# Kernel optimization log

Hardware: AMD Instinct MI355X
Metric: run time of the kernel (lower is better)

The kernel has to match this reference:

```python
import jax, jax.numpy as jnp
import numpy as np

B, N, D, H, E, K = 8, 1024, 768, 12, 4, 9
PAD = (K - 1) // 2


def _ln(x, g, b, eps=1e-5):
    m = jnp.mean(x, -1, keepdims=True)
    v = jnp.var(x, -1, keepdims=True)
    return (x - m) * jax.lax.rsqrt(v + eps) * g + b


def setup_inputs() -> dict:
    key = jax.random.key(0)
    ks = jax.random.split(key, 12)
    w = lambda k, s: jax.random.normal(k, s, jnp.float32) * 0.02
    return {
        "x": jax.random.normal(ks[0], (B, N, D), jnp.float32),
        "ff1_ln_g": jnp.ones(D), "ff1_ln_b": jnp.zeros(D),
        "ff1_w1": w(ks[1], (D, E * D)), "ff1_b1": jnp.zeros(E * D),
        "ff1_w2": w(ks[2], (E * D, D)), "ff1_b2": jnp.zeros(D),
        "attn_ln_g": jnp.ones(D), "attn_ln_b": jnp.zeros(D),
        "qkv_w": w(ks[3], (D, 3 * D)), "qkv_b": jnp.zeros(3 * D),
        "proj_w": w(ks[4], (D, D)), "proj_b": jnp.zeros(D),
        "rel_table": w(ks[5], (2 * N - 1, H)),
        "conv_ln_g": jnp.ones(D), "conv_ln_b": jnp.zeros(D),
        "pwin_w": w(ks[6], (2 * D, D)), "pwin_b": jnp.zeros(2 * D),
        "dw_w": w(ks[7], (D, 1, K)), "dw_b": jnp.zeros(D),
        "bn_g": jnp.ones(D), "bn_b": jnp.zeros(D),
        "pwout_w": w(ks[8], (D, D)), "pwout_b": jnp.zeros(D),
        "ff2_ln_g": jnp.ones(D), "ff2_ln_b": jnp.zeros(D),
        "ff2_w1": w(ks[9], (D, E * D)), "ff2_b1": jnp.zeros(E * D),
        "ff2_w2": w(ks[10], (E * D, D)), "ff2_b2": jnp.zeros(D),
        "fin_ln_g": jnp.ones(D), "fin_ln_b": jnp.zeros(D),
    }


def _ffn(x, g, b, w1, b1, w2, b2):
    h = jax.nn.gelu(_ln(x, g, b) @ w1 + b1, approximate=False)
    return h @ w2 + b2


def _attn(x, qkv_w, qkv_b, proj_w, proj_b, rel_table):
    b_, n_, c = x.shape
    hd = c // H
    qkv = (x @ qkv_w + qkv_b).reshape(b_, n_, 3, H, hd).transpose(2, 0, 3, 1, 4)
    q, k, v = qkv[0], qkv[1], qkv[2]  # (B, H, N, hd)
    scores = jnp.einsum('bhqd,bhkd->bhqk', q, k) * (hd ** -0.5)
    coords = jnp.arange(n_)
    idx = coords[None, :] - coords[:, None] + N - 1  # (N, N) in [0, 2N-2]
    bias = rel_table[idx].transpose(2, 0, 1)  # (H, N, N)
    a = jax.nn.softmax(scores + bias[None], axis=-1)
    out = jnp.einsum('bhqk,bhkd->bhqd', a, v).transpose(0, 2, 1, 3).reshape(b_, n_, c)
    return out @ proj_w + proj_b


def _conv(x, g, b, pwin_w, pwin_b, dw_w, dw_b, bn_g, bn_b, pwout_w, pwout_b):
    y = _ln(x, g, b) @ pwin_w.T + pwin_b  # pointwise-in conv as matmul -> (B, N, 2D)
    u, gate = jnp.split(y, 2, axis=-1)
    y = (u * jax.nn.sigmoid(gate)).transpose(0, 2, 1)  # GLU over channels -> (B, D, N)
    y = jax.lax.conv_general_dilated(
        y, dw_w, (1,), [(PAD, PAD)], feature_group_count=D,
        dimension_numbers=('NCH', 'OIH', 'NCH')) + dw_b[None, :, None]
    m = jnp.mean(y, (0, 2), keepdims=True)  # BatchNorm1d, training-mode batch stats
    v = jnp.var(y, (0, 2), keepdims=True)
    y = (y - m) * jax.lax.rsqrt(v + 1e-5) * bn_g[None, :, None] + bn_b[None, :, None]
    y = y * jax.nn.sigmoid(y)  # SiLU
    y = jnp.einsum('bcn,oc->bno', y, pwout_w) + pwout_b  # pointwise-out, back to (B, N, D)
    return y


def reference(x, ff1_ln_g, ff1_ln_b, ff1_w1, ff1_b1, ff1_w2, ff1_b2,
              attn_ln_g, attn_ln_b, qkv_w, qkv_b, proj_w, proj_b, rel_table,
              conv_ln_g, conv_ln_b, pwin_w, pwin_b, dw_w, dw_b, bn_g, bn_b,
              pwout_w, pwout_b, ff2_ln_g, ff2_ln_b, ff2_w1, ff2_b1, ff2_w2, ff2_b2,
              fin_ln_g, fin_ln_b):
    x = x + 0.5 * _ffn(x, ff1_ln_g, ff1_ln_b, ff1_w1, ff1_b1, ff1_w2, ff1_b2)
    x = x + _attn(_ln(x, attn_ln_g, attn_ln_b), qkv_w, qkv_b, proj_w, proj_b, rel_table)
    x = x + _conv(x, conv_ln_g, conv_ln_b, pwin_w, pwin_b, dw_w, dw_b, bn_g, bn_b, pwout_w, pwout_b)
    x = x + 0.5 * _ffn(x, ff2_ln_g, ff2_ln_b, ff2_w1, ff2_b1, ff2_w2, ff2_b2)
    return _ln(x, fin_ln_g, fin_ln_b)
```

## Files before the change

### kernel.cpp

```cpp
#include <hip/hip_runtime.h>
#include <math.h>

#define Bb 8
#define Nn 1024
#define Dd 768
#define Hh 12
#define Mm 8192

typedef __attribute__((ext_vector_type(4))) float f32x4;
typedef __attribute__((ext_vector_type(8))) __bf16 bf16x8;

__device__ __forceinline__ float bf2f(unsigned short u) {
  union { unsigned int i; float f; } v; v.i = ((unsigned int)u) << 16; return v.f;
}
__device__ __forceinline__ unsigned short f2bf(float f) {
  union { float f; unsigned int i; } v; v.f = f;
  unsigned int u = v.i;
  return (unsigned short)((u + 0x7FFFu + ((u >> 16) & 1u)) >> 16);
}
__device__ __forceinline__ unsigned int pack2bf(float a, float b) {
  union { __bf16 h[2]; unsigned int u; } x;
  x.h[0] = (__bf16)a; x.h[1] = (__bf16)b; return x.u;
}

__device__ __forceinline__ void gload16(const void* g, void* l) {
  __builtin_amdgcn_global_load_lds(
      (const __attribute__((address_space(1))) unsigned int*)g,
      (__attribute__((address_space(3))) unsigned int*)l, 16, 0, 0);
}

__device__ __forceinline__ float gelu_f(float v) {
  const float z = fabsf(v) * 0.7071067811865475f;
  const float t = __builtin_amdgcn_rcpf(1.f + 0.3275911f * z);
  const float poly = t*(0.254829592f + t*(-0.284496736f + t*(1.421413741f +
                     t*(-1.453152027f + t*1.061405429f))));
  float er = 1.f - poly * __expf(-z * z);
  er = copysignf(er, v);
  return 0.5f * v * (1.f + er);
}

template<int EPI, int NT>
__global__ __launch_bounds__(256)
void gemm_bt(const unsigned short* __restrict__ A,
             const unsigned short* __restrict__ Bt,
             const float* __restrict__ bias,
             unsigned short* __restrict__ Cbf,
             float* __restrict__ Res,
             const float* __restrict__ Xin,
             unsigned short* __restrict__ Vtr,
             int M, int N, int K, float scale)
{
  __shared__ __align__(16) unsigned short Asm[128*64];
  __shared__ __align__(16) unsigned short Bsm[NT*64];
  const int tid = threadIdx.x;
  const int wv = tid >> 6, lane = tid & 63;
  const int lr = lane & 15, lg = lane >> 4;
  const int wr = wv >> 1, wc = wv & 1;
  constexpr int JN = NT / 32;

  const int gx = gridDim.x, gy = gridDim.y;
  const int nwg = gx * gy;
  const int lin = blockIdx.y * gx + blockIdx.x;
  const int q8 = nwg >> 3, r8 = nwg & 7;
  const int xcd = lin & 7, lidx = lin >> 3;
  const int wg = ((xcd < r8) ? xcd * (q8 + 1) : r8 * (q8 + 1) + (xcd - r8) * q8) + lidx;
  const int bx = wg % gx;
  const int by = wg / gx;

  const int n0 = bx * NT, m0 = by * 128;

  f32x4 acc[4][JN] = {};

  const int srow8 = lane >> 3;
  const int scol  = ((lane & 7) ^ srow8) * 8;
  const unsigned short* Agp = A + (size_t)(m0 + wv*32 + srow8)*K + scol;
  const unsigned short* Bgp = (NT == 128)
      ? Bt + (size_t)(n0 + wv*32 + srow8)*K + scol
      : Bt + (size_t)(n0 + wv*16 + srow8)*K + scol;
  const int swr = (lr & 7) << 4;

  for (int kt = 0; kt < K; kt += 64) {
#pragma unroll
    for (int k = 0; k < 4; k++)
      gload16(Agp + (size_t)(k*8)*K + kt, Asm + (wv*32 + k*8)*64);
    if (NT == 128) {
#pragma unroll
      for (int k = 0; k < 4; k++)
        gload16(Bgp + (size_t)(k*8)*K + kt, Bsm + (wv*32 + k*8)*64);
    } else {
#pragma unroll
      for (int k = 0; k < 2; k++)
        gload16(Bgp + (size_t)(k*8)*K + kt, Bsm + (wv*16 + k*8)*64);
    }
    __syncthreads();
    bf16x8 af[4], af2[4], bfr[JN], bfr2[JN];
#pragma unroll
    for (int i = 0; i < 4; i++) {
      const char* base = (const char*)Asm + (wr*64 + i*16 + lr)*128;
      af[i]  = *(const bf16x8*)(base + ((lg*16)      ^ swr));
      af2[i] = *(const bf16x8*)(base + ((lg*16 + 64) ^ swr));
    }
#pragma unroll
    for (int j = 0; j < JN; j++) {
      const char* base = (const char*)Bsm + (wc*(NT/2) + j*16 + lr)*128;
      bfr[j]  = *(const bf16x8*)(base + ((lg*16)      ^ swr));
      bfr2[j] = *(const bf16x8*)(base + ((lg*16 + 64) ^ swr));
    }
#pragma unroll
    for (int i = 0; i < 4; i++)
#pragma unroll
      for (int j = 0; j < JN; j++) {
        acc[i][j] = __builtin_amdgcn_mfma_f32_16x16x32_bf16(af[i],  bfr[j],  acc[i][j], 0, 0, 0);
        acc[i][j] = __builtin_amdgcn_mfma_f32_16x16x32_bf16(af2[i], bfr2[j], acc[i][j], 0, 0, 0);
      }
    __syncthreads();
  }

#pragma unroll
  for (int i = 0; i < 4; i++) {
    const int rg = m0 + wr*64 + i*16 + lg*4;
    if (EPI == 3) {
#pragma unroll
      for (int j = 0; j < JN; j += 2) {
        const int cgu = n0 + wc*(NT/2) + j*16 + lr;
        const float bu = bias[cgu], bg = bias[cgu + 16];
        const int ocol = (n0 >> 1) + wc*(NT/4) + (j >> 1)*16 + lr;
#pragma unroll
        for (int e = 0; e < 4; e++) {
          float u  = acc[i][j][e]   + bu;
          float gt = acc[i][j+1][e] + bg;
          Cbf[(size_t)(rg + e) * (N >> 1) + ocol] = f2bf(u / (1.f + __expf(-gt)));
        }
      }
    } else if (EPI == 5 && n0 >= 1536) {
#pragma unroll
      for (int j = 0; j < JN; j++) {
        const int cg = n0 + wc*(NT/2) + j*16 + lr;
        const float bv = bias[cg];
        const int vo = cg - 1536;
        const int hh = vo >> 6, d = vo & 63;
        const int bb_ = rg >> 10, nn_ = rg & 1023;
        ushort4 o4;
        o4.x = f2bf(acc[i][j][0] + bv);
        o4.y = f2bf(acc[i][j][1] + bv);
        o4.z = f2bf(acc[i][j][2] + bv);
        o4.w = f2bf(acc[i][j][3] + bv);
        *(ushort4*)(Vtr + (((size_t)bb_*Hh + hh)*64 + d)*1024 + nn_) = o4;
      }
    } else {
#pragma unroll
      for (int j = 0; j < JN; j++) {
        const int cg = n0 + wc*(NT/2) + j*16 + lr;
        const float bv = bias[cg];
#pragma unroll
        for (int e = 0; e < 4; e++) {
          float v = acc[i][j][e] + bv;
          const size_t idx = (size_t)(rg + e) * N + cg;
          if (EPI == 1) {
            Cbf[idx] = f2bf(gelu_f(v));
          } else if (EPI == 0 || EPI == 5) {
            Cbf[idx] = f2bf(v);
          } else if (EPI == 2) {
            Res[idx] += scale * v;
          } else {
            Res[idx] = Xin[idx] + scale * v;
          }
        }
      }
    }
  }
}

template<bool OBF>
__global__ __launch_bounds__(256)
void ln_kernel(const float* x, const float* __restrict__ g,
               const float* __restrict__ b, void* out)
{
  const int row = blockIdx.x, tid = threadIdx.x;
  const float* xr = x + (size_t)row * Dd;
  float v0 = xr[tid], v1 = xr[tid+256], v2 = xr[tid+512];
  float s = v0+v1+v2, q = v0*v0+v1*v1+v2*v2;
  for (int off = 32; off; off >>= 1) { s += __shfl_down(s, off); q += __shfl_down(q, off); }
  __shared__ float ps[4], pq[4];
  if ((tid & 63) == 0) { ps[tid>>6] = s; pq[tid>>6] = q; }
  __syncthreads();
  s = ps[0]+ps[1]+ps[2]+ps[3]; q = pq[0]+pq[1]+pq[2]+pq[3];
  const float mean = s * (1.f/768.f);
  const float rstd = rsqrtf(q*(1.f/768.f) - mean*mean + 1e-5f);
  float y0 = (v0-mean)*rstd*g[tid]     + b[tid];
  float y1 = (v1-mean)*rstd*g[tid+256] + b[tid+256];
  float y2 = (v2-mean)*rstd*g[tid+512] + b[tid+512];
  if (OBF) {
    unsigned short* o = (unsigned short*)out + (size_t)row * Dd;
    o[tid] = f2bf(y0); o[tid+256] = f2bf(y1); o[tid+512] = f2bf(y2);
  } else {
    float* o = (float*)out + (size_t)row * Dd;
    o[tid] = y0; o[tid+256] = y1; o[tid+512] = y2;
  }
}

__global__ __launch_bounds__(256)
void transpose_w(const float* __restrict__ src, unsigned short* __restrict__ dst,
                 int K, int N)
{
  __shared__ float t[32][33];
  const int tx = threadIdx.x, ty = threadIdx.y;
  const int n0 = blockIdx.x * 32, k0 = blockIdx.y * 32;
#pragma unroll
  for (int i = 0; i < 4; i++) t[ty + i*8][tx] = src[(size_t)(k0 + ty + i*8)*N + n0 + tx];
  __syncthreads();
#pragma unroll
  for (int i = 0; i < 4; i++)
    dst[(size_t)(n0 + ty + i*8)*K + k0 + tx] = f2bf(t[tx][ty + i*8]);
}

__global__ __launch_bounds__(256)
void convert_bf(const float* __restrict__ src, unsigned short* __restrict__ dst, int n)
{
  for (int i = blockIdx.x*256 + threadIdx.x; i < n; i += gridDim.x*256)
    dst[i] = f2bf(src[i]);
}

__global__ __launch_bounds__(256)
void perm_pwin(const float* __restrict__ w, const float* __restrict__ b,
               unsigned short* __restrict__ wt, float* __restrict__ bperm)
{
  const int r = blockIdx.x;
  const int blk = r >> 7, g = (r >> 4) & 7, t = r & 15;
  const int orig = blk*64 + ((g >> 1) << 4) + t + ((g & 1) ? 768 : 0);
  const float* src = w + (size_t)orig * 768;
  unsigned short* dst = wt + (size_t)r * 768;
  const int tid = threadIdx.x;
  dst[tid] = f2bf(src[tid]); dst[tid+256] = f2bf(src[tid+256]); dst[tid+512] = f2bf(src[tid+512]);
  if (tid == 0) bperm[r] = b[orig];
}

__global__ __launch_bounds__(256)
void dw_tr(const float* __restrict__ src, float* __restrict__ dst)
{
  const int id = blockIdx.x*256 + threadIdx.x;
  if (id >= 9*768) return;
  const int k = id / 768, d = id % 768;
  dst[id] = src[d*9 + k];
}

__global__ __launch_bounds__(256)
void attn_kernel(const unsigned short* __restrict__ qkv,
                 const unsigned short* __restrict__ vtr,
                 const float* __restrict__ rel,
                 unsigned short* __restrict__ out)
{
  const int bh = blockIdx.x; const int b = bh / Hh, h = bh % Hh;
  const int q0 = blockIdx.y * 64;
  const int tid = threadIdx.x, wv = tid >> 6, lane = tid & 63;
  const int lr = lane & 15, lg = lane >> 4;

  __shared__ __align__(16) unsigned short Kl[64*72];
  __shared__ __align__(16) unsigned short Vt[64*72 + 64];
  __shared__ __align__(16) unsigned short Pl[4*16*72];
  __shared__ float relh[2048];

  for (int i = tid; i < 2047; i += 256) relh[i] = rel[(size_t)i*Hh + h] * 1.44269504f;

  const size_t qrow = (size_t)(b*Nn + q0 + wv*16 + lr);
  const bf16x8 qraw0 = *(const bf16x8*)(qkv + qrow*2304 + h*64 + lg*8);
  const bf16x8 qraw1 = *(const bf16x8*)(qkv + qrow*2304 + h*64 + 32 + lg*8);
  bf16x8 qf0, qf1;
#pragma unroll
  for (int e = 0; e < 8; e++) {
    qf0[e] = (__bf16)((float)qraw0[e] * 0.180336884f);
    qf1[e] = (__bf16)((float)qraw1[e] * 0.180336884f);
  }

  const int sd = tid >> 2;
  const int sc = (tid & 3) * 16;
  unsigned short* Pw = Pl + wv*16*72;

  const unsigned short* kbase = qkv + (size_t)(b*Nn + sd)*2304 + 768 + h*64 + sc;
  const unsigned short* vbase = vtr + ((size_t)bh*64 + sd)*Nn + sc;
  bf16x8 kA = *(const bf16x8*)(kbase);
  bf16x8 kB = *(const bf16x8*)(kbase + 8);
  bf16x8 vA = *(const bf16x8*)(vbase);
  bf16x8 vB = *(const bf16x8*)(vbase + 8);

  f32x4 O[4] = {};
  float mrow = -1e30f, lsum = 0.f;
  const int qq = q0 + wv*16 + lr;

  __syncthreads();

  for (int kt = 0; kt < Nn; kt += 64) {
    {
      *(bf16x8*)&Kl[sd*72 + sc]     = kA;
      *(bf16x8*)&Kl[sd*72 + sc + 8] = kB;
      const int vb_ = sd*72 + (sd>>4)*16 + sc;
      *(bf16x8*)&Vt[vb_]     = vA;
      *(bf16x8*)&Vt[vb_ + 8] = vB;
    }
    __syncthreads();

    if (kt + 64 < Nn) {
      const unsigned short* kn = kbase + (size_t)(kt + 64)*2304;
      const unsigned short* vn = vbase + (kt + 64);
      kA = *(const bf16x8*)(kn);
      kB = *(const bf16x8*)(kn + 8);
      vA = *(const bf16x8*)(vn);
      vB = *(const bf16x8*)(vn + 8);
    }

    f32x4 s[4] = {};
#pragma unroll
    for (int kb = 0; kb < 4; kb++) {
      bf16x8 kfa = *(const bf16x8*)&Kl[(kb*16 + lr)*72 + lg*8];
      bf16x8 kfb = *(const bf16x8*)&Kl[(kb*16 + lr)*72 + 32 + lg*8];
      s[kb] = __builtin_amdgcn_mfma_f32_16x16x32_bf16(kfa, qf0, s[kb], 0, 0, 0);
      s[kb] = __builtin_amdgcn_mfma_f32_16x16x32_bf16(kfb, qf1, s[kb], 0, 0, 0);
    }

    const int bidx = kt - qq + (Nn - 1);
    float v[4][4]; float r = -1e30f;
#pragma unroll
    for (int kb = 0; kb < 4; kb++)
#pragma unroll
      for (int j = 0; j < 4; j++) {
        float t = s[kb][j] + relh[bidx + kb*16 + lg*4 + j];
        v[kb][j] = t; r = fmaxf(r, t);
      }
    r = fmaxf(r, __shfl_xor(r, 16)); r = fmaxf(r, __shfl_xor(r, 32));

    if (!__all(r <= mrow + 11.5f)) {
      const float mn = fmaxf(mrow, r);
      const float al = __builtin_amdgcn_exp2f(mrow - mn);
      mrow = mn;
      lsum *= al;
#pragma unroll
      for (int ni = 0; ni < 4; ni++) {
        O[ni][0]*=al; O[ni][1]*=al; O[ni][2]*=al; O[ni][3]*=al;
      }
    }

    float rs = 0.f;
    unsigned int pk[8];
#pragma unroll
    for (int kb = 0; kb < 4; kb++) {
      float p0 = __builtin_amdgcn_exp2f(v[kb][0]-mrow), p1 = __builtin_amdgcn_exp2f(v[kb][1]-mrow);
      float p2 = __builtin_amdgcn_exp2f(v[kb][2]-mrow), p3 = __builtin_amdgcn_exp2f(v[kb][3]-mrow);
      rs += (p0+p1) + (p2+p3);
      pk[kb*2]   = pack2bf(p0, p1);
      pk[kb*2+1] = pack2bf(p2, p3);
    }
    rs += __shfl_xor(rs, 16); rs += __shfl_xor(rs, 32);
    lsum += rs;

#pragma unroll
    for (int kb0 = 0; kb0 < 4; kb0++) {
      const int kb = (kb0 + lg) & 3;
      *(unsigned int*)&Pw[lr*72 + kb*16 + lg*4]     = pk[kb*2];
      *(unsigned int*)&Pw[lr*72 + kb*16 + lg*4 + 2] = pk[kb*2+1];
    }

    bf16x8 pf0 = *(const bf16x8*)&Pw[lr*72 + lg*8];
    bf16x8 pf1 = *(const bf16x8*)&Pw[lr*72 + 32 + lg*8];
#pragma unroll
    for (int dt = 0; dt < 4; dt++) {
      bf16x8 vf0 = *(const bf16x8*)&Vt[(dt*16 + lr)*72 + dt*16 + lg*8];
      bf16x8 vf1 = *(const bf16x8*)&Vt[(dt*16 + lr)*72 + dt*16 + 32 + lg*8];
      O[dt] = __builtin_amdgcn_mfma_f32_16x16x32_bf16(vf0, pf0, O[dt], 0, 0, 0);
      O[dt] = __builtin_amdgcn_mfma_f32_16x16x32_bf16(vf1, pf1, O[dt], 0, 0, 0);
    }
    __syncthreads();
  }

  const float rl = 1.f / lsum;
#pragma unroll
  for (int dt = 0; dt < 4; dt++) {
    ushort4 o4;
    o4.x = f2bf(O[dt][0]*rl); o4.y = f2bf(O[dt][1]*rl);
    o4.z = f2bf(O[dt][2]*rl); o4.w = f2bf(O[dt][3]*rl);
    *(ushort4*)(out + (size_t)(b*Nn + qq)*Dd + h*64 + dt*16 + lg*4) = o4;
  }
}

__global__ __launch_bounds__(256)
void dwconv(const unsigned short* __restrict__ glu, const float* __restrict__ dwwT,
            const float* __restrict__ dwb, unsigned short* __restrict__ z)
{
  const int id = blockIdx.x*256 + threadIdx.x;
  if (id >= Mm*96) return;
  const int row = id / 96, c8 = (id % 96) * 8;
  const int n = row % Nn;
  float acc[8] = {};
#pragma unroll
  for (int k = 0; k < 9; k++) {
    const int nn = n + k - 4;
    if (nn >= 0 && nn < Nn) {
      bf16x8 gv = *(const bf16x8*)&glu[(size_t)(row + k - 4)*768 + c8];
      const float4 w0 = *(const float4*)&dwwT[k*768 + c8];
      const float4 w1 = *(const float4*)&dwwT[k*768 + c8 + 4];
      acc[0] += w0.x*(float)gv[0]; acc[1] += w0.y*(float)gv[1];
      acc[2] += w0.z*(float)gv[2]; acc[3] += w0.w*(float)gv[3];
      acc[4] += w1.x*(float)gv[4]; acc[5] += w1.y*(float)gv[5];
      acc[6] += w1.z*(float)gv[6]; acc[7] += w1.w*(float)gv[7];
    }
  }
  bf16x8 o;
#pragma unroll
  for (int e = 0; e < 8; e++) o[e] = (__bf16)(acc[e] + dwb[c8+e]);
  *(bf16x8*)&z[(size_t)row*768 + c8] = o;
}

__global__ __launch_bounds__(192)
void bn_part(const unsigned short* __restrict__ z, float* __restrict__ psum,
             float* __restrict__ psq)
{
  const int blk = blockIdx.x, t = threadIdx.x;
  const int c4 = t * 4;
  float s0=0,s1=0,s2=0,s3=0, q0=0,q1=0,q2=0,q3=0;
  for (int r = 0; r < 128; r++) {
    ushort4 v4 = *(const ushort4*)&z[(size_t)(blk*128 + r)*Dd + c4];
    float a = bf2f(v4.x), b_ = bf2f(v4.y), c = bf2f(v4.z), d = bf2f(v4.w);
    s0 += a; s1 += b_; s2 += c; s3 += d;
    q0 += a*a; q1 += b_*b_; q2 += c*c; q3 += d*d;
  }
  float4 sv = {s0, s1, s2, s3}, qv = {q0, q1, q2, q3};
  *(float4*)&psum[(size_t)blk*Dd + c4] = sv;
  *(float4*)&psq [(size_t)blk*Dd + c4] = qv;
}

__global__ __launch_bounds__(256)
void bn_final(const float* __restrict__ psum, const float* __restrict__ psq,
              const float* __restrict__ g, const float* __restrict__ bb,
              float* __restrict__ scale, float* __restrict__ shift)
{
  const int c = blockIdx.x*256 + threadIdx.x;
  if (c >= Dd) return;
  float s = 0.f, q = 0.f;
  for (int i = 0; i < 64; i++) { s += psum[(size_t)i*Dd + c]; q += psq[(size_t)i*Dd + c]; }
  const float mean = s / (float)Mm;
  const float var  = q / (float)Mm - mean*mean;
  const float sc = g[c] * rsqrtf(var + 1e-5f);
  scale[c] = sc; shift[c] = bb[c] - mean*sc;
}

__global__ __launch_bounds__(256)
void bn_silu(const unsigned short* __restrict__ z, const float* __restrict__ scale,
             const float* __restrict__ shift, unsigned short* __restrict__ out)
{
  const int id = blockIdx.x*256 + threadIdx.x;
  if (id >= Mm*96) return;
  const int row = id / 96, c8 = (id % 96) * 8;
  bf16x8 v = *(const bf16x8*)&z[(size_t)row*Dd + c8];
  bf16x8 o;
#pragma unroll
  for (int e = 0; e < 8; e++) {
    float t = (float)v[e] * scale[c8+e] + shift[c8+e];
    o[e] = (__bf16)(t / (1.f + __expf(-t)));
  }
  *(bf16x8*)&out[(size_t)row*Dd + c8] = o;
}

extern "C" void kernel_launch(void* const* d_in, const int* in_sizes, int n_in,
                              void* d_out, int out_size, void* d_ws, size_t ws_size,
                              hipStream_t stream)
{
  const float* x        = (const float*)d_in[0];
  const float* ff1_ln_g = (const float*)d_in[1];
  const float* ff1_ln_b = (const float*)d_in[2];
  const float* ff1_w1   = (const float*)d_in[3];
  const float* ff1_b1   = (const float*)d_in[4];
  const float* ff1_w2   = (const float*)d_in[5];
  const float* ff1_b2   = (const float*)d_in[6];
  const float* attn_ln_g= (const float*)d_in[7];
  const float* attn_ln_b= (const float*)d_in[8];
  const float* qkv_w    = (const float*)d_in[9];
  const float* qkv_b    = (const float*)d_in[10];
  const float* proj_w   = (const float*)d_in[11];
  const float* proj_b   = (const float*)d_in[12];
  const float* rel_tab  = (const float*)d_in[13];
  const float* conv_ln_g= (const float*)d_in[14];
  const float* conv_ln_b= (const float*)d_in[15];
  const float* pwin_w   = (const float*)d_in[16];
  const float* pwin_b   = (const float*)d_in[17];
  const float* dw_w     = (const float*)d_in[18];
  const float* dw_b     = (const float*)d_in[19];
  const float* bn_g     = (const float*)d_in[20];
  const float* bn_b     = (const float*)d_in[21];
  const float* pwout_w  = (const float*)d_in[22];
  const float* pwout_b  = (const float*)d_in[23];
  const float* ff2_ln_g = (const float*)d_in[24];
  const float* ff2_ln_b = (const float*)d_in[25];
  const float* ff2_w1   = (const float*)d_in[26];
  const float* ff2_b1   = (const float*)d_in[27];
  const float* ff2_w2   = (const float*)d_in[28];
  const float* ff2_b2   = (const float*)d_in[29];
  const float* fin_ln_g = (const float*)d_in[30];
  const float* fin_ln_b = (const float*)d_in[31];

  char* ws = (char*)d_ws;
  size_t off = 0;
  auto alloc = [&](size_t bytes) { char* p = ws + off; off += (bytes + 255) & ~(size_t)255; return p; };
  unsigned short* wt_ff1_1 = (unsigned short*)alloc((size_t)3072*768*2);
  unsigned short* wt_ff1_2 = (unsigned short*)alloc((size_t)768*3072*2);
  unsigned short* wt_qkv   = (unsigned short*)alloc((size_t)2304*768*2);
  unsigned short* wt_proj  = (unsigned short*)alloc((size_t)768*768*2);
  unsigned short* wt_pwin  = (unsigned short*)alloc((size_t)1536*768*2);
  unsigned short* wt_pwout = (unsigned short*)alloc((size_t)768*768*2);
  unsigned short* wt_ff2_1 = (unsigned short*)alloc((size_t)3072*768*2);
  unsigned short* wt_ff2_2 = (unsigned short*)alloc((size_t)768*3072*2);
  unsigned short* ybf      = (unsigned short*)alloc((size_t)Mm*768*2);
  unsigned short* big      = (unsigned short*)alloc((size_t)Mm*3072*2);
  unsigned short* abuf     = (unsigned short*)alloc((size_t)Mm*768*2);
  float* psum    = (float*)alloc((size_t)64*768*4);
  float* psq     = (float*)alloc((size_t)64*768*4);
  float* bnscale = (float*)alloc((size_t)768*4);
  float* bnshift = (float*)alloc((size_t)768*4);
  float* dwwT    = (float*)alloc((size_t)9*768*4);
  float* bperm   = (float*)alloc((size_t)1536*4);
  if (off > ws_size) return;

  unsigned short* vtr = big + (size_t)Mm*2304;

  float* xres = (float*)d_out;
  const dim3 tb(256);

  transpose_w<<<dim3(3072/32, 768/32), dim3(32,8), 0, stream>>>(ff1_w1, wt_ff1_1, 768, 3072);
  transpose_w<<<dim3(768/32, 3072/32), dim3(32,8), 0, stream>>>(ff1_w2, wt_ff1_2, 3072, 768);
  transpose_w<<<dim3(2304/32, 768/32), dim3(32,8), 0, stream>>>(qkv_w,  wt_qkv,  768, 2304);
  transpose_w<<<dim3(768/32, 768/32),  dim3(32,8), 0, stream>>>(proj_w, wt_proj, 768, 768);
  transpose_w<<<dim3(3072/32, 768/32), dim3(32,8), 0, stream>>>(ff2_w1, wt_ff2_1, 768, 3072);
  transpose_w<<<dim3(768/32, 3072/32), dim3(32,8), 0, stream>>>(ff2_w2, wt_ff2_2, 3072, 768);
  perm_pwin<<<1536, tb, 0, stream>>>(pwin_w, pwin_b, wt_pwin, bperm);
  convert_bf<<<2048, tb, 0, stream>>>(pwout_w, wt_pwout, 768*768);
  dw_tr<<<27, tb, 0, stream>>>(dw_w, dwwT);

  ln_kernel<true><<<Mm, tb, 0, stream>>>(x, ff1_ln_g, ff1_ln_b, ybf);
  gemm_bt<1,128><<<dim3(3072/128, Mm/128), tb, 0, stream>>>(ybf, wt_ff1_1, ff1_b1, big, nullptr, nullptr, nullptr, Mm, 3072, 768, 0.f);
  gemm_bt<4,64><<<dim3(768/64, Mm/128), tb, 0, stream>>>(big, wt_ff1_2, ff1_b2, nullptr, xres, x, nullptr, Mm, 768, 3072, 0.5f);

  ln_kernel<true><<<Mm, tb, 0, stream>>>(xres, attn_ln_g, attn_ln_b, ybf);
  gemm_bt<5,128><<<dim3(2304/128, Mm/128), tb, 0, stream>>>(ybf, wt_qkv, qkv_b, big, nullptr, nullptr, vtr, Mm, 2304, 768, 0.f);
  attn_kernel<<<dim3(Bb*Hh, Nn/64), tb, 0, stream>>>(big, vtr, rel_tab, abuf);
  gemm_bt<2,64><<<dim3(768/64, Mm/128), tb, 0, stream>>>(abuf, wt_proj, proj_b, nullptr, xres, nullptr, nullptr, Mm, 768, 768, 1.0f);

  ln_kernel<true><<<Mm, tb, 0, stream>>>(xres, conv_ln_g, conv_ln_b, ybf);
  gemm_bt<3,128><<<dim3(1536/128, Mm/128), tb, 0, stream>>>(ybf, wt_pwin, bperm, abuf, nullptr, nullptr, nullptr, Mm, 1536, 768, 0.f);
  dwconv<<<(Mm*96)/256, tb, 0, stream>>>(abuf, dwwT, dw_b, ybf);
  bn_part<<<64, dim3(192), 0, stream>>>(ybf, psum, psq);
  bn_final<<<3, tb, 0, stream>>>(psum, psq, bn_g, bn_b, bnscale, bnshift);
  bn_silu<<<(Mm*96)/256, tb, 0, stream>>>(ybf, bnscale, bnshift, abuf);
  gemm_bt<2,64><<<dim3(768/64, Mm/128), tb, 0, stream>>>(abuf, wt_pwout, pwout_b, nullptr, xres, nullptr, nullptr, Mm, 768, 768, 1.0f);

  ln_kernel<true><<<Mm, tb, 0, stream>>>(xres, ff2_ln_g, ff2_ln_b, ybf);
  gemm_bt<1,128><<<dim3(3072/128, Mm/128), tb, 0, stream>>>(ybf, wt_ff2_1, ff2_b1, big, nullptr, nullptr, nullptr, Mm, 3072, 768, 0.f);
  gemm_bt<2,64><<<dim3(768/64, Mm/128), tb, 0, stream>>>(big, wt_ff2_2, ff2_b2, nullptr, xres, nullptr, nullptr, Mm, 768, 3072, 0.5f);

  ln_kernel<false><<<Mm, tb, 0, stream>>>(xres, fin_ln_g, fin_ln_b, (void*)xres);
}
```

Before: 558.0 us.

## Load V fragments directly from global memory and fold rel bias into MFMA accumulator

Drops the shared-memory V tile and its register prefetch. Each wave now reads its V MFMA fragments straight from the transposed V buffer in global memory (L2/L1 cached), which removes LDS stores and frees shared memory for higher occupancy. The relative-position bias is also preloaded into the score accumulator before the QK MFMAs, so the separate add pass goes away. The risk is that V loads are no longer prefetched and now sit on the critical path before the PV MFMAs, and each of the four waves reads the same V tile redundantly.

```diff
diff --git a/kernel.cpp b/kernel.cpp
--- a/kernel.cpp
+++ b/kernel.cpp
@@ -256,7 +256,6 @@
   const int lr = lane & 15, lg = lane >> 4;
 
   __shared__ __align__(16) unsigned short Kl[64*72];
-  __shared__ __align__(16) unsigned short Vt[64*72 + 64];
   __shared__ __align__(16) unsigned short Pl[4*16*72];
   __shared__ float relh[2048];
 
@@ -277,11 +276,9 @@
   unsigned short* Pw = Pl + wv*16*72;
 
   const unsigned short* kbase = qkv + (size_t)(b*Nn + sd)*2304 + 768 + h*64 + sc;
-  const unsigned short* vbase = vtr + ((size_t)bh*64 + sd)*Nn + sc;
   bf16x8 kA = *(const bf16x8*)(kbase);
   bf16x8 kB = *(const bf16x8*)(kbase + 8);
-  bf16x8 vA = *(const bf16x8*)(vbase);
-  bf16x8 vB = *(const bf16x8*)(vbase + 8);
+  const unsigned short* vbase = vtr + ((size_t)bh*64 + lr)*1024 + lg*8;
 
   f32x4 O[4] = {};
   float mrow = -1e30f, lsum = 0.f;
@@ -290,25 +287,23 @@
   __syncthreads();
 
   for (int kt = 0; kt < Nn; kt += 64) {
-    {
-      *(bf16x8*)&Kl[sd*72 + sc]     = kA;
-      *(bf16x8*)&Kl[sd*72 + sc + 8] = kB;
-      const int vb_ = sd*72 + (sd>>4)*16 + sc;
-      *(bf16x8*)&Vt[vb_]     = vA;
-      *(bf16x8*)&Vt[vb_ + 8] = vB;
-    }
+    *(bf16x8*)&Kl[sd*72 + sc]     = kA;
+    *(bf16x8*)&Kl[sd*72 + sc + 8] = kB;
     __syncthreads();
 
     if (kt + 64 < Nn) {
       const unsigned short* kn = kbase + (size_t)(kt + 64)*2304;
-      const unsigned short* vn = vbase + (kt + 64);
       kA = *(const bf16x8*)(kn);
       kB = *(const bf16x8*)(kn + 8);
-      vA = *(const bf16x8*)(vn);
-      vB = *(const bf16x8*)(vn + 8);
-    }
-
-    f32x4 s[4] = {};
+    }
+
+    const int bidx = kt - qq + (Nn - 1);
+    f32x4 s[4];
+#pragma unroll
+    for (int kb = 0; kb < 4; kb++)
+#pragma unroll
+      for (int j = 0; j < 4; j++)
+        s[kb][j] = relh[bidx + kb*16 + lg*4 + j];
 #pragma unroll
     for (int kb = 0; kb < 4; kb++) {
       bf16x8 kfa = *(const bf16x8*)&Kl[(kb*16 + lr)*72 + lg*8];
@@ -317,15 +312,11 @@
       s[kb] = __builtin_amdgcn_mfma_f32_16x16x32_bf16(kfb, qf1, s[kb], 0, 0, 0);
     }
 
-    const int bidx = kt - qq + (Nn - 1);
-    float v[4][4]; float r = -1e30f;
+    float r = -1e30f;
 #pragma unroll
     for (int kb = 0; kb < 4; kb++)
 #pragma unroll
-      for (int j = 0; j < 4; j++) {
-        float t = s[kb][j] + relh[bidx + kb*16 + lg*4 + j];
-        v[kb][j] = t; r = fmaxf(r, t);
-      }
+      for (int j = 0; j < 4; j++) r = fmaxf(r, s[kb][j]);
     r = fmaxf(r, __shfl_xor(r, 16)); r = fmaxf(r, __shfl_xor(r, 32));
 
     if (!__all(r <= mrow + 11.5f)) {
@@ -343,8 +334,8 @@
     unsigned int pk[8];
 #pragma unroll
     for (int kb = 0; kb < 4; kb++) {
-      float p0 = __builtin_amdgcn_exp2f(v[kb][0]-mrow), p1 = __builtin_amdgcn_exp2f(v[kb][1]-mrow);
-      float p2 = __builtin_amdgcn_exp2f(v[kb][2]-mrow), p3 = __builtin_amdgcn_exp2f(v[kb][3]-mrow);
+      float p0 = __builtin_amdgcn_exp2f(s[kb][0]-mrow), p1 = __builtin_amdgcn_exp2f(s[kb][1]-mrow);
+      float p2 = __builtin_amdgcn_exp2f(s[kb][2]-mrow), p3 = __builtin_amdgcn_exp2f(s[kb][3]-mrow);
       rs += (p0+p1) + (p2+p3);
       pk[kb*2]   = pack2bf(p0, p1);
       pk[kb*2+1] = pack2bf(p2, p3);
@@ -363,8 +354,9 @@
     bf16x8 pf1 = *(const bf16x8*)&Pw[lr*72 + 32 + lg*8];
 #pragma unroll
     for (int dt = 0; dt < 4; dt++) {
-      bf16x8 vf0 = *(const bf16x8*)&Vt[(dt*16 + lr)*72 + dt*16 + lg*8];
-      bf16x8 vf1 = *(const bf16x8*)&Vt[(dt*16 + lr)*72 + dt*16 + 32 + lg*8];
+      const unsigned short* vp = vbase + (size_t)dt*16*1024 + kt;
+      bf16x8 vf0 = *(const bf16x8*)(vp);
+      bf16x8 vf1 = *(const bf16x8*)(vp + 32);
       O[dt] = __builtin_amdgcn_mfma_f32_16x16x32_bf16(vf0, pf0, O[dt], 0, 0, 0);
       O[dt] = __builtin_amdgcn_mfma_f32_16x16x32_bf16(vf1, pf1, O[dt], 0, 0, 0);
     }
```

Result: slower. 584.0 us (+4.7%).
